# Kernel tuning notes

Hardware: AMD Instinct MI355X
Metric: run time of the kernel (lower is better)

Reference implementation:

```python
import jax, jax.numpy as jnp
import numpy as np

BATCH, N_NODES = 256, 128
NF = MF = 128
EF = AEF = 5


def setup_inputs() -> dict:
    key = jax.random.key(0)
    k = jax.random.split(key, 6)
    afm = jax.random.normal(k[0], (BATCH, N_NODES, NF), dtype=jnp.float32)
    bfm = jax.random.randint(k[1], (BATCH, N_NODES, N_NODES), 0, EF + 1, dtype=jnp.int32)
    a_bfm = jax.random.randint(k[2], (BATCH, N_NODES), 0, AEF + 1, dtype=jnp.int32)
    adj = jax.random.uniform(k[3], (BATCH, N_NODES, N_NODES), dtype=jnp.float32)
    # xavier_uniform for adj_w (ef, mf, nf): fan_in=nf, fan_out=mf per torch convention on last two dims
    lim_w = float(np.sqrt(6.0 / (MF + NF)))
    adj_w = jax.random.uniform(k[4], (EF, MF, NF), minval=-lim_w, maxval=lim_w, dtype=jnp.float32)
    lim_a = float(np.sqrt(6.0 / (AEF + MF)))
    adj_a = jax.random.uniform(k[5], (AEF, MF), minval=-lim_a, maxval=lim_a, dtype=jnp.float32)
    return {"afm": afm, "bfm": bfm, "a_bfm": a_bfm, "adj": adj, "adj_w": adj_w, "adj_a": adj_a}


def reference(afm, bfm, a_bfm, adj, adj_w, adj_a):
    # afm is accepted by the original forward but never used.
    E = adj_w.shape[0] + 1  # zeros row for "no edge" at index 0
    mf, nf = adj_w.shape[1], adj_w.shape[2]
    W_ext = jnp.concatenate([jnp.zeros((1, mf, nf), adj_w.dtype), adj_w], axis=0)  # (E, mf, nf)
    A_ext = jnp.concatenate([jnp.zeros((1, mf), adj_a.dtype), adj_a], axis=0)      # (E_a, mf)
    att = A_ext[a_bfm]  # (b, n, mf); nf == mf required by original matmul
    # Original: msg[b,i,j,m] = sum_k W_ext[bfm[b,i,j], m, k] * att[b, j, k], then sum over i.
    # Contract first per edge type (small), then count-weight instead of gathering huge tensor.
    contrib = jnp.einsum('emn,bjn->bjem', W_ext, att)                  # (b, n, E, mf)
    cnt = jax.nn.one_hot(bfm, E, dtype=contrib.dtype).sum(axis=1)      # (b, j, E) = #{i : bfm[b,i,j]=e}
    messages = jnp.einsum('bje,bjem->bjm', cnt, contrib)               # (b, n, mf)
    return jnp.matmul(adj, messages)                                   # (b, n, mf)
```

## Files before the change

### kernel.cpp

```cpp
#include <hip/hip_runtime.h>

typedef short s16x8 __attribute__((ext_vector_type(8)));
typedef float f32x4 __attribute__((ext_vector_type(4)));

__device__ __forceinline__ short f2bf(float f) {
  union { float f; unsigned u; } cv;
  cv.f = f;
  unsigned u = cv.u;
  u = (u + 0x7FFFu + ((u >> 16) & 1u)) >> 16;
  return (short)u;
}
__device__ __forceinline__ unsigned pk2(float lo, float hi) {
  union { float f; unsigned u; } a, b;
  a.f = lo;
  b.f = hi;
  return (a.u >> 16) | (b.u & 0xFFFF0000u);
}

__global__ __launch_bounds__(256, 4) void hist_mc_kernel(
    const int* __restrict__ bfm, const float* __restrict__ adj_w,
    const float* __restrict__ adj_a, uint2* __restrict__ cnt_h,
    unsigned short* __restrict__ McT) {
  __shared__ unsigned red[4][32][4][2];
  __shared__ float As[5][128];
  const int t = threadIdx.x;

  if (blockIdx.x < 20) {
    const int bi = blockIdx.x;
    const int e = bi >> 2, mg = bi & 3;
    for (int idx = t; idx < 640; idx += 256) As[idx >> 7][idx & 127] = adj_a[idx];
    __syncthreads();
    const int m = mg * 32 + (t >> 3), ns = t & 7;
    const float* W = adj_w + (size_t)e * 16384 + (size_t)m * 128 + ns * 16;
    float acc[5] = {0.f, 0.f, 0.f, 0.f, 0.f};
#pragma unroll
    for (int it = 0; it < 4; ++it) {
      const float4 wv = *(const float4*)(W + it * 4);
      const float wa[4] = {wv.x, wv.y, wv.z, wv.w};
#pragma unroll
      for (int q = 0; q < 4; ++q) {
        const int n = ns * 16 + it * 4 + q;
#pragma unroll
        for (int a = 0; a < 5; ++a) acc[a] = fmaf(wa[q], As[a][n], acc[a]);
      }
    }
#pragma unroll
    for (int d = 1; d < 8; d <<= 1)
#pragma unroll
      for (int a = 0; a < 5; ++a) acc[a] += __shfl_xor(acc[a], d);
    if (ns == 0) {
#pragma unroll
      for (int a = 0; a < 5; ++a)
        McT[m * 40 + e * 5 + a] = (unsigned short)f2bf(acc[a]);
      if (e == 0)
#pragma unroll
        for (int r = 25; r < 40; ++r) McT[m * 40 + r] = 0;
    }
    return;
  }

  const int idx2 = blockIdx.x - 20;
  const int b = idx2 >> 1, hh = idx2 & 1;
  const int w = t >> 6, l = t & 63;
  const int4* bp = (const int4*)bfm + (size_t)b * 4096 + hh * 2048;
  unsigned pA[4] = {0, 0, 0, 0}, pB[4] = {0, 0, 0, 0};
#pragma unroll
  for (int it = 0; it < 8; ++it) {
    const int4 v = bp[it * 256 + t];
    const int vv[4] = {v.x, v.y, v.z, v.w};
#pragma unroll
    for (int jj = 0; jj < 4; ++jj) {
      pA[jj] += (unsigned)(vv[jj] == 1) + ((unsigned)(vv[jj] == 2) << 8) +
                ((unsigned)(vv[jj] == 3) << 16) + ((unsigned)(vv[jj] == 4) << 24);
      pB[jj] += (unsigned)(vv[jj] == 5);
    }
  }
#pragma unroll
  for (int jj = 0; jj < 4; ++jj) {
    pA[jj] += (unsigned)__shfl_xor((int)pA[jj], 32);
    pB[jj] += (unsigned)__shfl_xor((int)pB[jj], 32);
  }
  if (l < 32) {
#pragma unroll
    for (int jj = 0; jj < 4; ++jj) {
      red[w][l][jj][0] = pA[jj];
      red[w][l][jj][1] = pB[jj];
    }
  }
  __syncthreads();
  if (t < 128) {
    unsigned A = 0, B = 0;
    const int cc = t >> 2, jj = t & 3;
#pragma unroll
    for (int w2 = 0; w2 < 4; ++w2) {
      A += red[w2][cc][jj][0];
      B += red[w2][cc][jj][1];
    }
    cnt_h[(b * 2 + hh) * 128 + t] = make_uint2(A, B);
  }
}

__global__ __launch_bounds__(256, 2) void skinny_kernel(
    const float* __restrict__ adj, const int* __restrict__ a_bfm,
    const uint2* __restrict__ cnt_h, const unsigned short* __restrict__ McT,
    float* __restrict__ out) {
  __shared__ __align__(16) unsigned short Pt[32 * 128];
  __shared__ __align__(16) unsigned short Mt[128 * 40];
  __shared__ __align__(16) unsigned short Qs[4 * 16 * 40];
  const int bh = blockIdx.x, b = bh >> 1, hh = bh & 1;
  const int t = threadIdx.x, w = t >> 6, l = t & 63, g = l >> 4, c = l & 15;
  const int row0 = hh * 64 + w * 16;

  uint2 h0 = make_uint2(0u, 0u), h1 = make_uint2(0u, 0u);
  int av = 0;
  if (t < 128) {
    h0 = cnt_h[(b * 2 + 0) * 128 + t];
    h1 = cnt_h[(b * 2 + 1) * 128 + t];
    av = a_bfm[b * 128 + t];
  }
  s16x8 mst0 = *(const s16x8*)&McT[t * 8];
  s16x8 mst1 = *(const s16x8*)&McT[(256 + t) * 8];
  s16x8 mst2 = {0, 0, 0, 0, 0, 0, 0, 0};
  if (t < 128) mst2 = *(const s16x8*)&McT[(512 + t) * 8];
  const float* arow = adj + (size_t)b * 16384 + (size_t)(row0 + c) * 128;
  float4 a0[4], a1[4];
#pragma unroll
  for (int kk = 0; kk < 4; ++kk) {
    a0[kk] = *(const float4*)(arow + kk * 32 + g * 8);
    a1[kk] = *(const float4*)(arow + kk * 32 + g * 8 + 4);
  }

#pragma unroll
  for (int i = 0; i < 2; ++i)
    ((uint4*)Pt)[i * 256 + t] = make_uint4(0u, 0u, 0u, 0u);
  *(s16x8*)&Mt[t * 8] = mst0;
  *(s16x8*)&Mt[(256 + t) * 8] = mst1;
  if (t < 128) *(s16x8*)&Mt[(512 + t) * 8] = mst2;
  asm volatile("s_waitcnt lgkmcnt(0)" ::: "memory");
  __builtin_amdgcn_s_barrier();

  if (t < 128 && av > 0) {
    const unsigned cx = h0.x + h1.x;
    const unsigned cy = h0.y + h1.y;
    const int ai = av - 1;
    const int chunk = t >> 3, off = t & 7;
    const float cf[5] = {(float)(cx & 255u), (float)((cx >> 8) & 255u),
                         (float)((cx >> 16) & 255u), (float)(cx >> 24),
                         (float)(cy & 255u)};
#pragma unroll
    for (int ei = 0; ei < 5; ++ei) {
      const int r = ei * 5 + ai;
      Pt[r * 128 + ((chunk ^ (r & 15)) << 3) + off] =
          (unsigned short)f2bf(cf[ei]);
    }
  }
  asm volatile("s_waitcnt lgkmcnt(0)" ::: "memory");
  __builtin_amdgcn_s_barrier();

  s16x8 bP[4][2];
#pragma unroll
  for (int kk = 0; kk < 4; ++kk)
#pragma unroll
    for (int ct = 0; ct < 2; ++ct) {
      const int r = ct * 16 + c;
      bP[kk][ct] = *(const s16x8*)&Pt[r * 128 + (((kk * 4 + g) ^ (r & 15)) << 3)];
    }
  s16x8 apk[4];
#pragma unroll
  for (int kk = 0; kk < 4; ++kk) {
    unsigned* pu = (unsigned*)&apk[kk];
    pu[0] = pk2(a0[kk].x, a0[kk].y);
    pu[1] = pk2(a0[kk].z, a0[kk].w);
    pu[2] = pk2(a1[kk].x, a1[kk].y);
    pu[3] = pk2(a1[kk].z, a1[kk].w);
  }
  f32x4 accQ[2] = {{0.f, 0.f, 0.f, 0.f}, {0.f, 0.f, 0.f, 0.f}};
#pragma unroll
  for (int kk = 0; kk < 4; ++kk)
#pragma unroll
    for (int ct = 0; ct < 2; ++ct)
      accQ[ct] = __builtin_amdgcn_mfma_f32_16x16x32_bf16(apk[kk], bP[kk][ct],
                                                         accQ[ct], 0, 0, 0);

  unsigned short* qsw = &Qs[w * 16 * 40];
#pragma unroll
  for (int ct = 0; ct < 2; ++ct)
#pragma unroll
    for (int q = 0; q < 4; ++q)
      qsw[(g * 4 + q) * 40 + ct * 16 + c] = (unsigned short)f2bf(accQ[ct][q]);
  const s16x8 aQ = *(const s16x8*)&qsw[c * 40 + g * 8];

  float* ob = out + (size_t)b * 16384 + (size_t)row0 * 128;
#pragma unroll
  for (int mt = 0; mt < 8; ++mt) {
    const s16x8 bM = *(const s16x8*)&Mt[(mt * 16 + c) * 40 + g * 8];
    f32x4 acc2 = {0.f, 0.f, 0.f, 0.f};
    acc2 = __builtin_amdgcn_mfma_f32_16x16x32_bf16(aQ, bM, acc2, 0, 0, 0);
#pragma unroll
    for (int q = 0; q < 4; ++q)
      ob[(g * 4 + q) * 128 + mt * 16 + c] = acc2[q];
  }
}

extern "C" void kernel_launch(void* const* d_in, const int* in_sizes, int n_in,
                              void* d_out, int out_size, void* d_ws,
                              size_t ws_size, hipStream_t stream) {
  const int* bfm = (const int*)d_in[1];
  const int* a_bfm = (const int*)d_in[2];
  const float* adj = (const float*)d_in[3];
  const float* adj_w = (const float*)d_in[4];
  const float* adj_a = (const float*)d_in[5];
  float* out = (float*)d_out;

  unsigned short* McT = (unsigned short*)d_ws;
  uint2* cnt_h = (uint2*)((char*)d_ws + 16384);

  hist_mc_kernel<<<dim3(532), dim3(256), 0, stream>>>(bfm, adj_w, adj_a,
                                                      cnt_h, McT);
  skinny_kernel<<<dim3(512), dim3(256), 0, stream>>>(adj, a_bfm, cnt_h, McT,
                                                     out);
}
```

Before: 17.08 us.

## Fuse histogram into per-batch GEMM kernel and split McT precompute

Moves the bfm edge-type histogram into the main per-batch kernel, using 512-thread blocks that each cover one whole batch, so the counts no longer round-trip through global memory. The small McT precompute runs as its own lighter kernel with more blocks. The second MFMA swaps its operands so each lane writes a contiguous float4 of output instead of scattered scalars. The cost is fewer, larger blocks (256 instead of 512) and more registers held per thread for the prefetched bfm data.

After: 19.51 us. 14.2% more time.

```diff
diff --git a/kernel.cpp b/kernel.cpp
--- a/kernel.cpp
+++ b/kernel.cpp
@@ -17,57 +17,77 @@
   return (a.u >> 16) | (b.u & 0xFFFF0000u);
 }
 
-__global__ __launch_bounds__(256, 4) void hist_mc_kernel(
-    const int* __restrict__ bfm, const float* __restrict__ adj_w,
-    const float* __restrict__ adj_a, uint2* __restrict__ cnt_h,
+__global__ __launch_bounds__(256) void precomp_McT(
+    const float* __restrict__ adj_w, const float* __restrict__ adj_a,
     unsigned short* __restrict__ McT) {
-  __shared__ unsigned red[4][32][4][2];
   __shared__ float As[5][128];
   const int t = threadIdx.x;
+  const int e = blockIdx.x >> 4, mg = blockIdx.x & 15;
+  for (int idx = t; idx < 640; idx += 256) As[idx >> 7][idx & 127] = adj_a[idx];
+  __syncthreads();
+  const int m = mg * 8 + (t >> 5), l2 = t & 31;
+  const float4 wv = *(const float4*)(adj_w + (size_t)e * 16384 +
+                                     (size_t)m * 128 + l2 * 4);
+  const float wa[4] = {wv.x, wv.y, wv.z, wv.w};
+  float acc[5] = {0.f, 0.f, 0.f, 0.f, 0.f};
+#pragma unroll
+  for (int q = 0; q < 4; ++q) {
+    const int n = l2 * 4 + q;
+#pragma unroll
+    for (int a = 0; a < 5; ++a) acc[a] = fmaf(wa[q], As[a][n], acc[a]);
+  }
+#pragma unroll
+  for (int d = 1; d < 32; d <<= 1)
+#pragma unroll
+    for (int a = 0; a < 5; ++a) acc[a] += __shfl_xor(acc[a], d);
+  if (l2 == 0) {
+#pragma unroll
+    for (int a = 0; a < 5; ++a)
+      McT[m * 40 + e * 5 + a] = (unsigned short)f2bf(acc[a]);
+    if (e == 0)
+#pragma unroll
+      for (int r = 25; r < 40; ++r) McT[m * 40 + r] = 0;
+  }
+}
 
-  if (blockIdx.x < 20) {
-    const int bi = blockIdx.x;
-    const int e = bi >> 2, mg = bi & 3;
-    for (int idx = t; idx < 640; idx += 256) As[idx >> 7][idx & 127] = adj_a[idx];
-    __syncthreads();
-    const int m = mg * 32 + (t >> 3), ns = t & 7;
-    const float* W = adj_w + (size_t)e * 16384 + (size_t)m * 128 + ns * 16;
-    float acc[5] = {0.f, 0.f, 0.f, 0.f, 0.f};
+__global__ __launch_bounds__(512, 2) void fused_batch_kernel(
+    const int* __restrict__ bfm, const float* __restrict__ adj,
+    const int* __restrict__ a_bfm, const unsigned short* __restrict__ McT,
+    float* __restrict__ out) {
+  __shared__ unsigned red[8][32][4][2];
+  __shared__ __align__(16) unsigned short Pt[32 * 128];
+  __shared__ __align__(16) unsigned short Mt[128 * 40];
+  __shared__ __align__(16) unsigned short Qs[8 * 16 * 40];
+
+  const int b = blockIdx.x;
+  const int t = threadIdx.x, w = t >> 6, l = t & 63, g = l >> 4, c = l & 15;
+  const int row0 = w * 16;
+
+  const int4* bp = (const int4*)bfm + (size_t)b * 4096;
+  int4 bv[8];
 #pragma unroll
-    for (int it = 0; it < 4; ++it) {
-      const float4 wv = *(const float4*)(W + it * 4);
-      const float wa[4] = {wv.x, wv.y, wv.z, wv.w};
+  for (int it = 0; it < 8; ++it) bv[it] = bp[it * 512 + t];
+  s16x8 mst0 = *(const s16x8*)&McT[t * 8];
+  s16x8 mst1 = {0, 0, 0, 0, 0, 0, 0, 0};
+  if (t < 128) mst1 = *(const s16x8*)&McT[(512 + t) * 8];
+  int av = 0;
+  if (t < 128) av = a_bfm[b * 128 + t];
+  const float* arow = adj + (size_t)b * 16384 + (size_t)(row0 + c) * 128;
+  float4 a0[4], a1[4];
 #pragma unroll
-      for (int q = 0; q < 4; ++q) {
-        const int n = ns * 16 + it * 4 + q;
-#pragma unroll
-        for (int a = 0; a < 5; ++a) acc[a] = fmaf(wa[q], As[a][n], acc[a]);
-      }
-    }
-#pragma unroll
-    for (int d = 1; d < 8; d <<= 1)
-#pragma unroll
-      for (int a = 0; a < 5; ++a) acc[a] += __shfl_xor(acc[a], d);
-    if (ns == 0) {
-#pragma unroll
-      for (int a = 0; a < 5; ++a)
-        McT[m * 40 + e * 5 + a] = (unsigned short)f2bf(acc[a]);
-      if (e == 0)
-#pragma unroll
-        for (int r = 25; r < 40; ++r) McT[m * 40 + r] = 0;
-    }
-    return;
+  for (int kk = 0; kk < 4; ++kk) {
+    a0[kk] = *(const float4*)(arow + kk * 32 + g * 8);
+    a1[kk] = *(const float4*)(arow + kk * 32 + g * 8 + 4);
   }
 
-  const int idx2 = blockIdx.x - 20;
-  const int b = idx2 >> 1, hh = idx2 & 1;
-  const int w = t >> 6, l = t & 63;
-  const int4* bp = (const int4*)bfm + (size_t)b * 4096 + hh * 2048;
+#pragma unroll
+  for (int i = 0; i < 1; ++i)
+    ((uint4*)Pt)[t] = make_uint4(0u, 0u, 0u, 0u);
+
   unsigned pA[4] = {0, 0, 0, 0}, pB[4] = {0, 0, 0, 0};
 #pragma unroll
   for (int it = 0; it < 8; ++it) {
-    const int4 v = bp[it * 256 + t];
-    const int vv[4] = {v.x, v.y, v.z, v.w};
+    const int vv[4] = {bv[it].x, bv[it].y, bv[it].z, bv[it].w};
 #pragma unroll
     for (int jj = 0; jj < 4; ++jj) {
       pA[jj] += (unsigned)(vv[jj] == 1) + ((unsigned)(vv[jj] == 2) << 8) +
@@ -87,66 +107,24 @@
       red[w][l][jj][1] = pB[jj];
     }
   }
-  __syncthreads();
-  if (t < 128) {
-    unsigned A = 0, B = 0;
-    const int cc = t >> 2, jj = t & 3;
-#pragma unroll
-    for (int w2 = 0; w2 < 4; ++w2) {
-      A += red[w2][cc][jj][0];
-      B += red[w2][cc][jj][1];
-    }
-    cnt_h[(b * 2 + hh) * 128 + t] = make_uint2(A, B);
-  }
-}
-
-__global__ __launch_bounds__(256, 2) void skinny_kernel(
-    const float* __restrict__ adj, const int* __restrict__ a_bfm,
-    const uint2* __restrict__ cnt_h, const unsigned short* __restrict__ McT,
-    float* __restrict__ out) {
-  __shared__ __align__(16) unsigned short Pt[32 * 128];
-  __shared__ __align__(16) unsigned short Mt[128 * 40];
-  __shared__ __align__(16) unsigned short Qs[4 * 16 * 40];
-  const int bh = blockIdx.x, b = bh >> 1, hh = bh & 1;
-  const int t = threadIdx.x, w = t >> 6, l = t & 63, g = l >> 4, c = l & 15;
-  const int row0 = hh * 64 + w * 16;
-
-  uint2 h0 = make_uint2(0u, 0u), h1 = make_uint2(0u, 0u);
-  int av = 0;
-  if (t < 128) {
-    h0 = cnt_h[(b * 2 + 0) * 128 + t];
-    h1 = cnt_h[(b * 2 + 1) * 128 + t];
-    av = a_bfm[b * 128 + t];
-  }
-  s16x8 mst0 = *(const s16x8*)&McT[t * 8];
-  s16x8 mst1 = *(const s16x8*)&McT[(256 + t) * 8];
-  s16x8 mst2 = {0, 0, 0, 0, 0, 0, 0, 0};
-  if (t < 128) mst2 = *(const s16x8*)&McT[(512 + t) * 8];
-  const float* arow = adj + (size_t)b * 16384 + (size_t)(row0 + c) * 128;
-  float4 a0[4], a1[4];
-#pragma unroll
-  for (int kk = 0; kk < 4; ++kk) {
-    a0[kk] = *(const float4*)(arow + kk * 32 + g * 8);
-    a1[kk] = *(const float4*)(arow + kk * 32 + g * 8 + 4);
-  }
-
-#pragma unroll
-  for (int i = 0; i < 2; ++i)
-    ((uint4*)Pt)[i * 256 + t] = make_uint4(0u, 0u, 0u, 0u);
   *(s16x8*)&Mt[t * 8] = mst0;
-  *(s16x8*)&Mt[(256 + t) * 8] = mst1;
-  if (t < 128) *(s16x8*)&Mt[(512 + t) * 8] = mst2;
+  if (t < 128) *(s16x8*)&Mt[(512 + t) * 8] = mst1;
   asm volatile("s_waitcnt lgkmcnt(0)" ::: "memory");
   __builtin_amdgcn_s_barrier();
 
   if (t < 128 && av > 0) {
-    const unsigned cx = h0.x + h1.x;
-    const unsigned cy = h0.y + h1.y;
+    unsigned A = 0, B = 0;
+    const int cc = t >> 2, jj = t & 3;
+#pragma unroll
+    for (int w2 = 0; w2 < 8; ++w2) {
+      A += red[w2][cc][jj][0];
+      B += red[w2][cc][jj][1];
+    }
     const int ai = av - 1;
     const int chunk = t >> 3, off = t & 7;
-    const float cf[5] = {(float)(cx & 255u), (float)((cx >> 8) & 255u),
-                         (float)((cx >> 16) & 255u), (float)(cx >> 24),
-                         (float)(cy & 255u)};
+    const float cf[5] = {(float)(A & 255u), (float)((A >> 8) & 255u),
+                         (float)((A >> 16) & 255u), (float)(A >> 24),
+                         (float)(B & 255u)};
 #pragma unroll
     for (int ei = 0; ei < 5; ++ei) {
       const int r = ei * 5 + ai;
@@ -190,15 +168,13 @@
       qsw[(g * 4 + q) * 40 + ct * 16 + c] = (unsigned short)f2bf(accQ[ct][q]);
   const s16x8 aQ = *(const s16x8*)&qsw[c * 40 + g * 8];
 
-  float* ob = out + (size_t)b * 16384 + (size_t)row0 * 128;
+  float* ob = out + (size_t)b * 16384 + (size_t)(row0 + c) * 128;
 #pragma unroll
   for (int mt = 0; mt < 8; ++mt) {
-    const s16x8 bM = *(const s16x8*)&Mt[(mt * 16 + c) * 40 + g * 8];
+    const s16x8 aM = *(const s16x8*)&Mt[(mt * 16 + c) * 40 + g * 8];
     f32x4 acc2 = {0.f, 0.f, 0.f, 0.f};
-    acc2 = __builtin_amdgcn_mfma_f32_16x16x32_bf16(aQ, bM, acc2, 0, 0, 0);
-#pragma unroll
-    for (int q = 0; q < 4; ++q)
-      ob[(g * 4 + q) * 128 + mt * 16 + c] = acc2[q];
+    acc2 = __builtin_amdgcn_mfma_f32_16x16x32_bf16(aM, aQ, acc2, 0, 0, 0);
+    *(f32x4*)(ob + mt * 16 + g * 4) = acc2;
   }
 }
 
@@ -213,10 +189,8 @@
   float* out = (float*)d_out;
 
   unsigned short* McT = (unsigned short*)d_ws;
-  uint2* cnt_h = (uint2*)((char*)d_ws + 16384);
 
-  hist_mc_kernel<<<dim3(532), dim3(256), 0, stream>>>(bfm, adj_w, adj_a,
-                                                      cnt_h, McT);
-  skinny_kernel<<<dim3(512), dim3(256), 0, stream>>>(adj, a_bfm, cnt_h, McT,
-                                                     out);
+  precomp_McT<<<dim3(80), dim3(256), 0, stream>>>(adj_w, adj_a, McT);
+  fused_batch_kernel<<<dim3(256), dim3(512), 0, stream>>>(bfm, adj, a_bfm,
+                                                          McT, out);
 }
```
